# Kernel tuning notes

Hardware: AMD Instinct MI355X
Metric: run time of the kernel (lower is better)

The kernel has to match this reference:

```python
import jax, jax.numpy as jnp
import numpy as np


def _bilerp(grid, x, y):
    """Bilinear sample grid [H,W,C] at continuous coords x,y [B,V] -> [B,V,C]."""
    H, W = grid.shape[0], grid.shape[1]
    x0f = jnp.floor(x); y0f = jnp.floor(y)
    wx = (x - x0f)[..., None]; wy = (y - y0f)[..., None]
    x0 = jnp.clip(x0f.astype(jnp.int32), 0, W - 1)
    x1 = jnp.clip(x0f.astype(jnp.int32) + 1, 0, W - 1)
    y0 = jnp.clip(y0f.astype(jnp.int32), 0, H - 1)
    y1 = jnp.clip(y0f.astype(jnp.int32) + 1, 0, H - 1)
    return (grid[y0, x0] * (1 - wx) * (1 - wy) + grid[y0, x1] * wx * (1 - wy)
            + grid[y1, x0] * (1 - wx) * wy + grid[y1, x1] * wx * wy)


def _normalize(x, eps=1e-12):
    n = jnp.linalg.norm(x, axis=-1, keepdims=True)
    return x / jnp.maximum(n, eps)


def setup_inputs() -> dict:
    key = jax.random.key(0)
    ks = jax.random.split(key, 12)
    B, H, W = 4, 512, 512
    V, F = 100000, 200000
    return {
        "vertices": jax.random.normal(ks[0], (1, V, 3), jnp.float32),
        "vertices_texcoords": jax.random.uniform(ks[1], (1, V, 2), jnp.float32),
        "vertices_normals": jax.random.normal(ks[2], (1, V, 3), jnp.float32),
        "faces_vt_idx": jax.random.randint(ks[3], (1, F, 3), 0, V, jnp.int32),
        "faces_vn_idx": jax.random.randint(ks[4], (1, F, 3), 0, V, jnp.int32),
        "faces_v_idx": jax.random.randint(ks[5], (1, F, 3), 0, V, jnp.int32),
        "pose": jax.random.normal(ks[6], (B, 4, 4), jnp.float32),
        "depth": jax.random.uniform(ks[7], (B, H, W), jnp.float32),
        "face_index_map": jax.random.randint(ks[8], (B, H, W), 0, F, jnp.int32),
        "weight_map": jax.random.uniform(ks[9], (B, H, W, 3), jnp.float32),
        "v_uvz": jax.random.uniform(ks[10], (B, V, 3), jnp.float32),
        # +0.5 keeps the z component (used as 1/z) away from zero
        "faces_v_uvz": jax.random.uniform(ks[11], (B, F, 3, 3), jnp.float32) + 0.5,
    }


def reference(vertices, vertices_texcoords, vertices_normals, faces_vt_idx,
              faces_vn_idx, faces_v_idx, pose, depth, face_index_map,
              weight_map, v_uvz, faces_v_uvz):
    B, H, W = depth.shape
    mesh_span = (vertices[0].max(axis=0) - vertices[0].min(axis=0)).max()

    # --- screen-space vertex coords + bilinear depth lookup (front mask) ---
    vx = (v_uvz[..., 0] * 0.5 + 0.5) * W                  # [B,V]
    vy = (1.0 - (v_uvz[..., 1] * 0.5 + 0.5)) * H          # [B,V]
    v_depth = _bilerp(depth[0][..., None], vx, vy)        # [B,V,1] (batch-0 depth, as in source)
    v_front_mask = (v_uvz[0, :, 2] - v_depth[0, :, 0] < mesh_span * 0.005)[None, :]

    # --- perspective-corrected barycentric weights ---
    fz = faces_v_uvz[..., 2]                              # [B,F,3]
    fz_map = jax.vmap(lambda f, idx: f[idx])(fz, face_index_map)  # [B,H,W,3]
    wmap = (1.0 / fz_map) * weight_map * depth[..., None] # [B,H,W,3]
    wmap = wmap[..., None]                                # [B,H,W,3,1]

    # --- uv map ---
    faces_vt = vertices_texcoords[0][faces_vt_idx[0]]     # [F,3,2]
    uv_map = (faces_vt[face_index_map] * wmap).sum(axis=-2)  # [B,H,W,2]
    uv_map = uv_map - jnp.floor(uv_map)

    # --- normal map (object + camera space) ---
    faces_vn = vertices_normals[0][faces_vn_idx[0]]       # [F,3,3]
    normal_map = _normalize((faces_vn[face_index_map] * wmap).sum(axis=-2))
    R = pose[:, :3, :3]
    t = pose[:, :3, -1]
    normal_map_cam = _normalize(jnp.einsum('bij,bhwj->bhwi', R, normal_map))

    # --- position map (object + camera space) ---
    faces_v = vertices[0][faces_v_idx[0]]                 # [F,3,3]
    position_map = (faces_v[face_index_map] * wmap).sum(axis=-2)
    position_map_cam = jnp.einsum('bij,bhwj->bhwi', R, position_map) + t[:, None, None, :]

    # Concatenate float map outputs into one tensor [B,H,W,14]
    out = jnp.concatenate([uv_map, normal_map, normal_map_cam,
                           position_map, position_map_cam], axis=-1)
    return out
```

## Files before the change

### kernel.cpp

```cpp
#include <hip/hip_runtime.h>
#include <stdint.h>


struct H2 { _Float16 x, y; };
static __device__ __forceinline__ float packh(float a, float b) {
    H2 h; h.x = (_Float16)a; h.y = (_Float16)b;
    return __builtin_bit_cast(float, h);
}
static __device__ __forceinline__ float2 unph(float w) {
    H2 h = __builtin_bit_cast(H2, w);
    return make_float2((float)h.x, (float)h.y);
}

__global__ __launch_bounds__(256) void pack_faces(
    const float* __restrict__ tc, const float* __restrict__ nrm,
    const float* __restrict__ vtx,
    const int* __restrict__ f_vt, const int* __restrict__ f_vn,
    const int* __restrict__ f_v,
    float* __restrict__ rec, int F, int V)
{
    int f = blockIdx.x * 256 + threadIdx.x;
    if (f >= F) return;
    float w[16];
    float h[18];
#pragma unroll
    for (int k = 0; k < 3; ++k) {
        int ivt = f_vt[f * 3 + k];
        ivt = ivt < 0 ? 0 : (ivt >= V ? V - 1 : ivt);
        w[k * 2 + 0] = tc[(long)ivt * 2 + 0];
        w[k * 2 + 1] = tc[(long)ivt * 2 + 1];
        int ivn = f_vn[f * 3 + k];
        ivn = ivn < 0 ? 0 : (ivn >= V ? V - 1 : ivn);
        h[k * 3 + 0] = nrm[(long)ivn * 3 + 0];
        h[k * 3 + 1] = nrm[(long)ivn * 3 + 1];
        h[k * 3 + 2] = nrm[(long)ivn * 3 + 2];
        int iv = f_v[f * 3 + k];
        iv = iv < 0 ? 0 : (iv >= V ? V - 1 : iv);
        h[9 + k * 3 + 0] = vtx[(long)iv * 3 + 0];
        h[9 + k * 3 + 1] = vtx[(long)iv * 3 + 1];
        h[9 + k * 3 + 2] = vtx[(long)iv * 3 + 2];
    }
#pragma unroll
    for (int j = 0; j < 9; ++j)
        w[6 + j] = packh(h[2 * j], h[2 * j + 1]);
    w[15] = 0.0f;
    float4* o = (float4*)(rec + (long)f * 16);
#pragma unroll
    for (int j = 0; j < 4; ++j)
        o[j] = make_float4(w[j * 4], w[j * 4 + 1], w[j * 4 + 2], w[j * 4 + 3]);
}

__global__ __launch_bounds__(256) void pack_fz(
    const float* __restrict__ fuvz, float* __restrict__ fzq, long BF)
{
    long i = (long)blockIdx.x * 256 + threadIdx.x;
    if (i >= BF) return;
    const float* s = fuvz + i * 9;
    ((float4*)fzq)[i] = make_float4(__fdiv_rn(1.0f, s[2]),
                                    __fdiv_rn(1.0f, s[5]),
                                    __fdiv_rn(1.0f, s[8]), 0.0f);
}

__global__ __launch_bounds__(256) void raster_fast(
    const float* __restrict__ rec,
    const float* __restrict__ fzq,
    const float* __restrict__ pose,
    const float* __restrict__ depth,
    const int*   __restrict__ fim,
    const float* __restrict__ weight,
    float* __restrict__ out,
    int F, int HW)
{
    __shared__ float sb[256 * 14];
    const int tid = threadIdx.x;
    const int hw  = blockIdx.x * 256 + tid;
    const int b   = blockIdx.y;
    const int p   = b * HW + hw;

    const float* pb = pose + b * 16;
    float R00 = pb[0],  R01 = pb[1],  R02 = pb[2],  t0 = pb[3];
    float R10 = pb[4],  R11 = pb[5],  R12 = pb[6],  t1 = pb[7];
    float R20 = pb[8],  R21 = pb[9],  R22 = pb[10], t2 = pb[11];

    int f = fim[p];
    f = f < 0 ? 0 : (f >= F ? F - 1 : f);
    const float d = depth[p];
    float w0 = weight[(long)p * 3 + 0];
    float w1 = weight[(long)p * 3 + 1];
    float w2 = weight[(long)p * 3 + 2];

    const float4* R4 = (const float4*)(rec + (long)f * 16);
    float4 a0 = R4[0], a1 = R4[1], a2 = R4[2], a3 = R4[3];
    float4 fz = ((const float4*)fzq)[(long)b * F + f];

    float wm0 = __fmul_rn(__fmul_rn(fz.x, w0), d);
    float wm1 = __fmul_rn(__fmul_rn(fz.y, w1), d);
    float wm2 = __fmul_rn(__fmul_rn(fz.z, w2), d);

    float uv0 = __fadd_rn(__fadd_rn(__fmul_rn(a0.x, wm0), __fmul_rn(a0.z, wm1)),
                          __fmul_rn(a1.x, wm2));
    float uv1 = __fadd_rn(__fadd_rn(__fmul_rn(a0.y, wm0), __fmul_rn(a0.w, wm1)),
                          __fmul_rn(a1.y, wm2));
    uv0 -= floorf(uv0);
    uv1 -= floorf(uv1);

    float2 g0 = unph(a1.z), g1 = unph(a1.w), g2 = unph(a2.x);
    float2 g3 = unph(a2.y), g4 = unph(a2.z), g5 = unph(a2.w);
    float2 g6 = unph(a3.x), g7 = unph(a3.y), g8 = unph(a3.z);
    float n0 = g0.x * wm0 + g1.y * wm1 + g3.x * wm2;
    float n1 = g0.y * wm0 + g2.x * wm1 + g3.y * wm2;
    float n2 = g1.x * wm0 + g2.y * wm1 + g4.x * wm2;
    float p0 = g4.y * wm0 + g6.x * wm1 + g7.y * wm2;
    float p1 = g5.x * wm0 + g6.y * wm1 + g8.x * wm2;
    float p2 = g5.y * wm0 + g7.x * wm1 + g8.y * wm2;

    float nn = sqrtf(n0 * n0 + n1 * n1 + n2 * n2);
    float ni = 1.0f / fmaxf(nn, 1e-12f);
    float m0 = n0 * ni, m1 = n1 * ni, m2 = n2 * ni;

    float c0 = R00 * m0 + R01 * m1 + R02 * m2;
    float c1 = R10 * m0 + R11 * m1 + R12 * m2;
    float c2 = R20 * m0 + R21 * m1 + R22 * m2;
    float cn = sqrtf(c0 * c0 + c1 * c1 + c2 * c2);
    float ci = 1.0f / fmaxf(cn, 1e-12f);
    c0 *= ci; c1 *= ci; c2 *= ci;

    float q0 = R00 * p0 + R01 * p1 + R02 * p2 + t0;
    float q1 = R10 * p0 + R11 * p1 + R12 * p2 + t1;
    float q2 = R20 * p0 + R21 * p1 + R22 * p2 + t2;

    float* s = sb + tid * 14;
    s[0]  = uv0; s[1]  = uv1;
    s[2]  = m0;  s[3]  = m1;  s[4]  = m2;
    s[5]  = c0;  s[6]  = c1;  s[7]  = c2;
    s[8]  = p0;  s[9]  = p1;  s[10] = p2;
    s[11] = q0;  s[12] = q1;  s[13] = q2;
    __syncthreads();

    float4* og = (float4*)(out + ((long)b * HW + (long)blockIdx.x * 256) * 14);
    const float4* sv = (const float4*)sb;
#pragma unroll
    for (int j = 0; j < 4; ++j) {
        int k = tid + 256 * j;
        if (k < 896) og[k] = sv[k];
    }
}

__global__ __launch_bounds__(256) void raster_kernel(
    const float* __restrict__ vertices, const float* __restrict__ texcoords,
    const float* __restrict__ normals,
    const int* __restrict__ f_vt, const int* __restrict__ f_vn,
    const int* __restrict__ f_v,
    const float* __restrict__ pose, const float* __restrict__ depth,
    const int* __restrict__ fim, const float* __restrict__ weight,
    const float* __restrict__ fuvz, float* __restrict__ out, int F, int V,
    int HW)
{
    const int hw = blockIdx.x * 256 + threadIdx.x;
    if (hw >= HW) return;
    const int b  = blockIdx.y;
    const int p  = b * HW + hw;
    const float* pb = pose + b * 16;
    float R00 = pb[0], R01 = pb[1], R02 = pb[2],  t0 = pb[3];
    float R10 = pb[4], R11 = pb[5], R12 = pb[6],  t1 = pb[7];
    float R20 = pb[8], R21 = pb[9], R22 = pb[10], t2 = pb[11];
    int f = fim[p];
    f = f < 0 ? 0 : (f >= F ? F - 1 : f);
    const float d = depth[p];
    const float* fz = fuvz + ((long)b * F + f) * 9;
    float wm[3];
#pragma unroll
    for (int k = 0; k < 3; ++k)
        wm[k] = __fmul_rn(__fmul_rn(__fdiv_rn(1.0f, fz[k * 3 + 2]),
                                    weight[(long)p * 3 + k]), d);
    float u0t[3], u1t[3];
    float n0 = 0.f, n1 = 0.f, n2 = 0.f, p0 = 0.f, p1 = 0.f, p2 = 0.f;
#pragma unroll
    for (int k = 0; k < 3; ++k) {
        int ivt = f_vt[f * 3 + k], ivn = f_vn[f * 3 + k], iv = f_v[f * 3 + k];
        ivt = ivt < 0 ? 0 : (ivt >= V ? V - 1 : ivt);
        ivn = ivn < 0 ? 0 : (ivn >= V ? V - 1 : ivn);
        iv  = iv  < 0 ? 0 : (iv  >= V ? V - 1 : iv);
        const float* tc = texcoords + (long)ivt * 2;
        u0t[k] = __fmul_rn(tc[0], wm[k]);
        u1t[k] = __fmul_rn(tc[1], wm[k]);
        const float* nr = normals + (long)ivn * 3;
        n0 += nr[0] * wm[k]; n1 += nr[1] * wm[k]; n2 += nr[2] * wm[k];
        const float* vv = vertices + (long)iv * 3;
        p0 += vv[0] * wm[k]; p1 += vv[1] * wm[k]; p2 += vv[2] * wm[k];
    }
    float uv0 = __fadd_rn(__fadd_rn(u0t[0], u0t[1]), u0t[2]);
    float uv1 = __fadd_rn(__fadd_rn(u1t[0], u1t[1]), u1t[2]);
    uv0 -= floorf(uv0); uv1 -= floorf(uv1);
    float nn = sqrtf(n0 * n0 + n1 * n1 + n2 * n2);
    float ni = 1.0f / fmaxf(nn, 1e-12f);
    float m0 = n0 * ni, m1 = n1 * ni, m2 = n2 * ni;
    float c0 = R00 * m0 + R01 * m1 + R02 * m2;
    float c1 = R10 * m0 + R11 * m1 + R12 * m2;
    float c2 = R20 * m0 + R21 * m1 + R22 * m2;
    float cn = sqrtf(c0 * c0 + c1 * c1 + c2 * c2);
    float ci = 1.0f / fmaxf(cn, 1e-12f);
    c0 *= ci; c1 *= ci; c2 *= ci;
    float q0 = R00 * p0 + R01 * p1 + R02 * p2 + t0;
    float q1 = R10 * p0 + R11 * p1 + R12 * p2 + t1;
    float q2 = R20 * p0 + R21 * p1 + R22 * p2 + t2;
    float2* o = (float2*)(out + (long)p * 14);
    o[0] = make_float2(uv0, uv1); o[1] = make_float2(m0, m1);
    o[2] = make_float2(m2, c0);   o[3] = make_float2(c1, c2);
    o[4] = make_float2(p0, p1);   o[5] = make_float2(p2, q0);
    o[6] = make_float2(q1, q2);
}

extern "C" void kernel_launch(void* const* d_in, const int* in_sizes, int n_in,
                              void* d_out, int out_size, void* d_ws, size_t ws_size,
                              hipStream_t stream) {
    const float* vertices  = (const float*)d_in[0];
    const float* texcoords = (const float*)d_in[1];
    const float* normals   = (const float*)d_in[2];
    const int*   f_vt      = (const int*)  d_in[3];
    const int*   f_vn      = (const int*)  d_in[4];
    const int*   f_v       = (const int*)  d_in[5];
    const float* pose      = (const float*)d_in[6];
    const float* depth     = (const float*)d_in[7];
    const int*   fim       = (const int*)  d_in[8];
    const float* weight    = (const float*)d_in[9];
    const float* fuvz      = (const float*)d_in[11];
    float* out = (float*)d_out;

    const int B  = in_sizes[6] / 16;
    const int F  = in_sizes[3] / 3;
    const int V  = in_sizes[1] / 2;
    const int HW = in_sizes[7] / B;

    const size_t rec_bytes = (size_t)F * 64;
    const size_t fzq_bytes = (size_t)B * F * 16;
    const bool ws_ok = d_ws != nullptr &&
                       ws_size >= rec_bytes + fzq_bytes &&
                       (((uintptr_t)d_ws) & 15) == 0 &&
                       (HW % 256) == 0;

    if (ws_ok) {
        float* rec = (float*)d_ws;
        float* fzq = (float*)((char*)d_ws + rec_bytes);
        long BF = (long)B * F;
        pack_faces<<<(F + 255) / 256, 256, 0, stream>>>(
            texcoords, normals, vertices, f_vt, f_vn, f_v, rec, F, V);
        pack_fz<<<(unsigned)((BF + 255) / 256), 256, 0, stream>>>(fuvz, fzq, BF);
        dim3 grid(HW / 256, B);
        raster_fast<<<grid, 256, 0, stream>>>(
            rec, fzq, pose, depth, fim, weight, out, F, HW);
    } else {
        dim3 grid((HW + 255) / 256, B);
        raster_kernel<<<grid, 256, 0, stream>>>(
            vertices, texcoords, normals, f_vt, f_vn, f_v,
            pose, depth, fim, weight, fuvz, out, F, V, HW);
    }
}
```

Before: 177.0 us.

## Pre-pack vertex normals/positions to fp16 tables and coalesce staging through LDS

A new prep kernel converts per-vertex normals and positions into compact 8-byte fp16 tables. The same kernel computes the per-face reciprocal-z array, staging the 9-float face records through shared memory so global loads are coalesced. Face packing now gathers one 8-byte entry per vertex instead of three scattered floats, and writes its records through LDS for coalesced stores. The raster kernel stages the per-pixel weight triples through shared memory, and the half-precision layout is reordered to match. This adds an extra workspace requirement and two more block barriers in the raster kernel.

After: 173.1 us. 2.2% less time.

```diff
diff --git a/kernel.cpp b/kernel.cpp
--- a/kernel.cpp
+++ b/kernel.cpp
@@ -3,16 +3,105 @@
 
 
 struct H2 { _Float16 x, y; };
+static __device__ __forceinline__ uint32_t packh_u(float a, float b) {
+    H2 h; h.x = (_Float16)a; h.y = (_Float16)b;
+    return __builtin_bit_cast(uint32_t, h);
+}
 static __device__ __forceinline__ float packh(float a, float b) {
-    H2 h; h.x = (_Float16)a; h.y = (_Float16)b;
-    return __builtin_bit_cast(float, h);
+    return __builtin_bit_cast(float, packh_u(a, b));
+}
+static __device__ __forceinline__ float asf(uint32_t u) {
+    return __builtin_bit_cast(float, u);
 }
 static __device__ __forceinline__ float2 unph(float w) {
     H2 h = __builtin_bit_cast(H2, w);
     return make_float2((float)h.x, (float)h.y);
 }
 
-__global__ __launch_bounds__(256) void pack_faces(
+
+__global__ __launch_bounds__(256) void prep_fz(
+    const float* __restrict__ nrm, const float* __restrict__ vtx,
+    const float* __restrict__ fuvz,
+    uint2* __restrict__ nrmh, uint2* __restrict__ vtxh,
+    float4* __restrict__ fzq, int V, long BF)
+{
+    __shared__ float sf[2304];
+    const int tid = threadIdx.x;
+    const long base = (long)blockIdx.x * 256;
+    const long i = base + tid;
+
+    if (nrmh != nullptr && i < V) {
+        const float* n = nrm + i * 3;
+        const float* v = vtx + i * 3;
+        nrmh[i] = make_uint2(packh_u(n[0], n[1]), packh_u(n[2], 0.0f));
+        vtxh[i] = make_uint2(packh_u(v[0], v[1]), packh_u(v[2], 0.0f));
+    }
+
+    if (base + 256 <= BF) {
+        const float4* src = (const float4*)(fuvz + base * 9);
+        float4* d = (float4*)sf;
+        d[tid]       = src[tid];
+        d[tid + 256] = src[tid + 256];
+        if (tid < 64) d[tid + 512] = src[tid + 512];
+        __syncthreads();
+        fzq[i] = make_float4(__fdiv_rn(1.0f, sf[tid * 9 + 2]),
+                             __fdiv_rn(1.0f, sf[tid * 9 + 5]),
+                             __fdiv_rn(1.0f, sf[tid * 9 + 8]), 0.0f);
+    } else if (i < BF) {
+        const float* s = fuvz + i * 9;
+        fzq[i] = make_float4(__fdiv_rn(1.0f, s[2]),
+                             __fdiv_rn(1.0f, s[5]),
+                             __fdiv_rn(1.0f, s[8]), 0.0f);
+    }
+}
+
+__global__ __launch_bounds__(256) void pack_faces2(
+    const float* __restrict__ tc,
+    const uint2* __restrict__ nrmh, const uint2* __restrict__ vtxh,
+    const int* __restrict__ f_vt, const int* __restrict__ f_vn,
+    const int* __restrict__ f_v,
+    float4* __restrict__ rec, int F, int V)
+{
+    __shared__ float4 sw[1024];
+    const int tid  = threadIdx.x;
+    const int base = blockIdx.x * 256;
+    const int f    = base + tid;
+
+    if (f < F) {
+        float2 t[3]; uint2 N[3], Vv[3];
+#pragma unroll
+        for (int k = 0; k < 3; ++k) {
+            int ivt = f_vt[f * 3 + k];
+            ivt = ivt < 0 ? 0 : (ivt >= V ? V - 1 : ivt);
+            t[k] = ((const float2*)tc)[ivt];
+            int ivn = f_vn[f * 3 + k];
+            ivn = ivn < 0 ? 0 : (ivn >= V ? V - 1 : ivn);
+            N[k] = nrmh[ivn];
+            int iv = f_v[f * 3 + k];
+            iv = iv < 0 ? 0 : (iv >= V ? V - 1 : iv);
+            Vv[k] = vtxh[iv];
+        }
+        uint32_t w9  = (N[0].y  & 0xffffu) | (N[1].y  << 16);
+        uint32_t w10 = (N[2].y  & 0xffffu) | (Vv[0].y << 16);
+        uint32_t w14 = (Vv[1].y & 0xffffu) | (Vv[2].y << 16);
+        float4* o = sw + tid * 4;
+        o[0] = make_float4(t[0].x, t[0].y, t[1].x, t[1].y);
+        o[1] = make_float4(t[2].x, t[2].y, asf(N[0].x), asf(N[1].x));
+        o[2] = make_float4(asf(N[2].x), asf(w9), asf(w10), asf(Vv[0].x));
+        o[3] = make_float4(asf(Vv[1].x), asf(Vv[2].x), asf(w14), 0.0f);
+    }
+    __syncthreads();
+    const int valid  = F - base;
+    const int valid4 = (valid < 256 ? valid : 256) * 4;
+    float4* og = rec + (long)base * 4;
+#pragma unroll
+    for (int j = 0; j < 4; ++j) {
+        int k = tid + 256 * j;
+        if (k < valid4) og[k] = sw[k];
+    }
+}
+
+__global__ __launch_bounds__(256) void pack_faces_old(
     const float* __restrict__ tc, const float* __restrict__ nrm,
     const float* __restrict__ vtx,
     const int* __restrict__ f_vt, const int* __restrict__ f_vn,
@@ -21,49 +110,36 @@
 {
     int f = blockIdx.x * 256 + threadIdx.x;
     if (f >= F) return;
-    float w[16];
-    float h[18];
+    float t[6], n[9], v[9];
 #pragma unroll
     for (int k = 0; k < 3; ++k) {
         int ivt = f_vt[f * 3 + k];
         ivt = ivt < 0 ? 0 : (ivt >= V ? V - 1 : ivt);
-        w[k * 2 + 0] = tc[(long)ivt * 2 + 0];
-        w[k * 2 + 1] = tc[(long)ivt * 2 + 1];
+        t[k * 2 + 0] = tc[(long)ivt * 2 + 0];
+        t[k * 2 + 1] = tc[(long)ivt * 2 + 1];
         int ivn = f_vn[f * 3 + k];
         ivn = ivn < 0 ? 0 : (ivn >= V ? V - 1 : ivn);
-        h[k * 3 + 0] = nrm[(long)ivn * 3 + 0];
-        h[k * 3 + 1] = nrm[(long)ivn * 3 + 1];
-        h[k * 3 + 2] = nrm[(long)ivn * 3 + 2];
+        n[k * 3 + 0] = nrm[(long)ivn * 3 + 0];
+        n[k * 3 + 1] = nrm[(long)ivn * 3 + 1];
+        n[k * 3 + 2] = nrm[(long)ivn * 3 + 2];
         int iv = f_v[f * 3 + k];
         iv = iv < 0 ? 0 : (iv >= V ? V - 1 : iv);
-        h[9 + k * 3 + 0] = vtx[(long)iv * 3 + 0];
-        h[9 + k * 3 + 1] = vtx[(long)iv * 3 + 1];
-        h[9 + k * 3 + 2] = vtx[(long)iv * 3 + 2];
-    }
-#pragma unroll
-    for (int j = 0; j < 9; ++j)
-        w[6 + j] = packh(h[2 * j], h[2 * j + 1]);
-    w[15] = 0.0f;
+        v[k * 3 + 0] = vtx[(long)iv * 3 + 0];
+        v[k * 3 + 1] = vtx[(long)iv * 3 + 1];
+        v[k * 3 + 2] = vtx[(long)iv * 3 + 2];
+    }
     float4* o = (float4*)(rec + (long)f * 16);
-#pragma unroll
-    for (int j = 0; j < 4; ++j)
-        o[j] = make_float4(w[j * 4], w[j * 4 + 1], w[j * 4 + 2], w[j * 4 + 3]);
-}
-
-__global__ __launch_bounds__(256) void pack_fz(
-    const float* __restrict__ fuvz, float* __restrict__ fzq, long BF)
-{
-    long i = (long)blockIdx.x * 256 + threadIdx.x;
-    if (i >= BF) return;
-    const float* s = fuvz + i * 9;
-    ((float4*)fzq)[i] = make_float4(__fdiv_rn(1.0f, s[2]),
-                                    __fdiv_rn(1.0f, s[5]),
-                                    __fdiv_rn(1.0f, s[8]), 0.0f);
-}
-
-__global__ __launch_bounds__(256) void raster_fast(
-    const float* __restrict__ rec,
-    const float* __restrict__ fzq,
+    o[0] = make_float4(t[0], t[1], t[2], t[3]);
+    o[1] = make_float4(t[4], t[5], packh(n[0], n[1]), packh(n[3], n[4]));
+    o[2] = make_float4(packh(n[6], n[7]), packh(n[2], n[5]),
+                       packh(n[8], v[2]), packh(v[0], v[1]));
+    o[3] = make_float4(packh(v[3], v[4]), packh(v[6], v[7]),
+                       packh(v[5], v[8]), 0.0f);
+}
+
+__global__ __launch_bounds__(256) void raster_fast2(
+    const float4* __restrict__ rec,
+    const float4* __restrict__ fzq,
     const float* __restrict__ pose,
     const float* __restrict__ depth,
     const int*   __restrict__ fim,
@@ -75,7 +151,13 @@
     const int tid = threadIdx.x;
     const int hw  = blockIdx.x * 256 + tid;
     const int b   = blockIdx.y;
-    const int p   = b * HW + hw;
+    const long p  = (long)b * HW + hw;
+
+    {
+        const float4* wsrc =
+            (const float4*)(weight + ((long)b * HW + (long)blockIdx.x * 256) * 3);
+        if (tid < 192) ((float4*)sb)[tid] = wsrc[tid];
+    }
 
     const float* pb = pose + b * 16;
     float R00 = pb[0],  R01 = pb[1],  R02 = pb[2],  t0 = pb[3];
@@ -85,13 +167,16 @@
     int f = fim[p];
     f = f < 0 ? 0 : (f >= F ? F - 1 : f);
     const float d = depth[p];
-    float w0 = weight[(long)p * 3 + 0];
-    float w1 = weight[(long)p * 3 + 1];
-    float w2 = weight[(long)p * 3 + 2];
-
-    const float4* R4 = (const float4*)(rec + (long)f * 16);
+
+    const float4* R4 = rec + (long)f * 4;
     float4 a0 = R4[0], a1 = R4[1], a2 = R4[2], a3 = R4[3];
-    float4 fz = ((const float4*)fzq)[(long)b * F + f];
+    float4 fz = fzq[(long)b * F + f];
+
+    __syncthreads();
+    float w0 = sb[tid * 3 + 0];
+    float w1 = sb[tid * 3 + 1];
+    float w2 = sb[tid * 3 + 2];
+    __syncthreads();
 
     float wm0 = __fmul_rn(__fmul_rn(fz.x, w0), d);
     float wm1 = __fmul_rn(__fmul_rn(fz.y, w1), d);
@@ -104,15 +189,23 @@
     uv0 -= floorf(uv0);
     uv1 -= floorf(uv1);
 
-    float2 g0 = unph(a1.z), g1 = unph(a1.w), g2 = unph(a2.x);
-    float2 g3 = unph(a2.y), g4 = unph(a2.z), g5 = unph(a2.w);
-    float2 g6 = unph(a3.x), g7 = unph(a3.y), g8 = unph(a3.z);
-    float n0 = g0.x * wm0 + g1.y * wm1 + g3.x * wm2;
-    float n1 = g0.y * wm0 + g2.x * wm1 + g3.y * wm2;
-    float n2 = g1.x * wm0 + g2.y * wm1 + g4.x * wm2;
-    float p0 = g4.y * wm0 + g6.x * wm1 + g7.y * wm2;
-    float p1 = g5.x * wm0 + g6.y * wm1 + g8.x * wm2;
-    float p2 = g5.y * wm0 + g7.x * wm1 + g8.y * wm2;
+    float2 u6  = unph(a1.z);
+    float2 u7  = unph(a1.w);
+    float2 u8  = unph(a2.x);
+    float2 u9  = unph(a2.y);
+    float2 u10 = unph(a2.z);
+    float2 u11 = unph(a2.w);
+    float2 u12 = unph(a3.x);
+    float2 u13 = unph(a3.y);
+    float2 u14 = unph(a3.z);
+
+    float n0 = u6.x * wm0 + u7.x * wm1 + u8.x * wm2;
+    float n1 = u6.y * wm0 + u7.y * wm1 + u8.y * wm2;
+    float n2 = u9.x * wm0 + u9.y * wm1 + u10.x * wm2;
+
+    float p0 = u11.x * wm0 + u12.x * wm1 + u13.x * wm2;
+    float p1 = u11.y * wm0 + u12.y * wm1 + u13.y * wm2;
+    float p2 = u10.y * wm0 + u14.x * wm1 + u14.y * wm2;
 
     float nn = sqrtf(n0 * n0 + n1 * n1 + n2 * n2);
     float ni = 1.0f / fmaxf(nn, 1e-12f);
@@ -231,24 +324,43 @@
     const int F  = in_sizes[3] / 3;
     const int V  = in_sizes[1] / 2;
     const int HW = in_sizes[7] / B;
+    const long BF = (long)B * F;
 
     const size_t rec_bytes = (size_t)F * 64;
-    const size_t fzq_bytes = (size_t)B * F * 16;
-    const bool ws_ok = d_ws != nullptr &&
-                       ws_size >= rec_bytes + fzq_bytes &&
-                       (((uintptr_t)d_ws) & 15) == 0 &&
-                       (HW % 256) == 0;
-
-    if (ws_ok) {
+    const size_t fzq_bytes = (size_t)BF * 16;
+    const size_t tab_bytes = (size_t)V * 8;
+    const bool base_ok = d_ws != nullptr &&
+                         (((uintptr_t)d_ws) & 15) == 0 &&
+                         (HW % 256) == 0;
+    const bool ws_new = base_ok &&
+                        ws_size >= rec_bytes + fzq_bytes + 2 * tab_bytes;
+    const bool ws_old = base_ok && ws_size >= rec_bytes + fzq_bytes;
+
+    if (ws_new) {
+        float* rec  = (float*)d_ws;
+        float* fzq  = (float*)((char*)d_ws + rec_bytes);
+        uint2* nrmh = (uint2*)((char*)d_ws + rec_bytes + fzq_bytes);
+        uint2* vtxh = (uint2*)((char*)d_ws + rec_bytes + fzq_bytes + tab_bytes);
+        long nb = BF > (long)V ? BF : (long)V;
+        prep_fz<<<(unsigned)((nb + 255) / 256), 256, 0, stream>>>(
+            normals, vertices, fuvz, nrmh, vtxh, (float4*)fzq, V, BF);
+        pack_faces2<<<(F + 255) / 256, 256, 0, stream>>>(
+            texcoords, nrmh, vtxh, f_vt, f_vn, f_v, (float4*)rec, F, V);
+        dim3 grid(HW / 256, B);
+        raster_fast2<<<grid, 256, 0, stream>>>(
+            (const float4*)rec, (const float4*)fzq, pose, depth, fim, weight,
+            out, F, HW);
+    } else if (ws_old) {
         float* rec = (float*)d_ws;
         float* fzq = (float*)((char*)d_ws + rec_bytes);
-        long BF = (long)B * F;
-        pack_faces<<<(F + 255) / 256, 256, 0, stream>>>(
+        prep_fz<<<(unsigned)((BF + 255) / 256), 256, 0, stream>>>(
+            normals, vertices, fuvz, nullptr, nullptr, (float4*)fzq, V, BF);
+        pack_faces_old<<<(F + 255) / 256, 256, 0, stream>>>(
             texcoords, normals, vertices, f_vt, f_vn, f_v, rec, F, V);
-        pack_fz<<<(unsigned)((BF + 255) / 256), 256, 0, stream>>>(fuvz, fzq, BF);
         dim3 grid(HW / 256, B);
-        raster_fast<<<grid, 256, 0, stream>>>(
-            rec, fzq, pose, depth, fim, weight, out, F, HW);
+        raster_fast2<<<grid, 256, 0, stream>>>(
+            (const float4*)rec, (const float4*)fzq, pose, depth, fim, weight,
+            out, F, HW);
     } else {
         dim3 grid((HW + 255) / 256, B);
         raster_kernel<<<grid, 256, 0, stream>>>(
```
